# Performance work log

Hardware: AMD Instinct MI355X
Metric: run time of the kernel (lower is better)

The kernel has to match this reference:

```python
import jax, jax.numpy as jnp
import numpy as np

BLOCK = 16
N1, N2, RANK = 64, 64, 64
# E2M1 (NVFP4) representable magnitudes
_FP4_GRID = jnp.array([0.0, 0.5, 1.0, 1.5, 2.0, 3.0, 4.0, 6.0], dtype=jnp.float32)
_FP4_MIDS = (_FP4_GRID[1:] + _FP4_GRID[:-1]) / 2.0


def quantize_to_nvfp4(x, block_size=BLOCK):
    """Per-block (last dim, block_size=16) NVFP4 fake-quant: amax scale to 6.0, round to E2M1 grid, dequant."""
    shape = x.shape
    xb = x.reshape(shape[:-1] + (shape[-1] // block_size, block_size))
    amax = jnp.max(jnp.abs(xb), axis=-1, keepdims=True)
    scale = jnp.maximum(amax / 6.0, 1e-8)
    y = xb / scale
    idx = jnp.searchsorted(_FP4_MIDS, jnp.abs(y), side='right')  # nearest grid index
    q = _FP4_GRID[idx] * jnp.sign(y)
    return (q * scale).reshape(shape)


def setup_inputs() -> dict:
    key = jax.random.key(0)
    ks = jax.random.split(key, 6)
    B, S, n, m, r = 4, 2048, 4096, 4096, RANK
    return {
        'x': jax.random.normal(ks[0], (B, S, n), dtype=jnp.float32),
        'smooth_scale': jax.random.uniform(ks[1], (n,), dtype=jnp.float32, minval=0.2, maxval=2.0),
        'a_q': jax.random.normal(ks[2], (m, r), dtype=jnp.float32) * 0.05,
        'b_q': jax.random.normal(ks[3], (N1, r), dtype=jnp.float32) * 0.1,
        'c_q_t': jax.random.normal(ks[4], (r, N2), dtype=jnp.float32) * 0.1,
        'bias': jax.random.normal(ks[5], (m,), dtype=jnp.float32),
    }


def reference(x, smooth_scale, a_q, b_q, c_q_t, bias):
    # smooth + activation quant
    x_q = quantize_to_nvfp4(x * smooth_scale, BLOCK)
    # reshape (..., n) -> (..., n1, n2)
    x_3d = x_q.reshape(x.shape[:-1] + (N1, N2))
    # contract C: F.linear(x_3d, c_q_t) -> (..., n1, r)
    h1 = jnp.einsum('bsij,rj->bsir', x_3d, c_q_t)
    # contract B: (h1 * B).sum over n1 -> (..., r)
    h2 = jnp.einsum('bsir,ir->bsr', h1, b_q)
    # contract A: h2 @ A.T + bias -> (..., m)
    out = jnp.einsum('bsr,mr->bsm', h2, a_q) + bias
    return out
```

## Files before the change

kernel.cpp:

```cpp
#include <hip/hip_runtime.h>

typedef float f32x4 __attribute__((ext_vector_type(4)));
typedef short s16x8 __attribute__((ext_vector_type(8)));
typedef short s16x4 __attribute__((ext_vector_type(4)));
typedef unsigned short u16;

#define N_COLS 4096
#define RANK 64

__device__ __forceinline__ unsigned f_asuint(float f) { union { float f; unsigned u; } v; v.f = f; return v.u; }
__device__ __forceinline__ float f_asfloat(unsigned u) { union { unsigned u; float f; } v; v.u = u; return v.f; }
__device__ __forceinline__ short f2bf(float f) {
  unsigned u = f_asuint(f);
  return (short)((u + 0x7fffu + ((u >> 16) & 1u)) >> 16);
}

__device__ __forceinline__ void gload_lds16(const void* g, void* l) {
  __builtin_amdgcn_global_load_lds(
      (const __attribute__((address_space(1))) unsigned int*)g,
      (__attribute__((address_space(3))) unsigned int*)l,
      16, 0, 0);
}

__global__ __launch_bounds__(256) void k_prep(const float* __restrict__ b_q,
                                              const float* __restrict__ c_q_t,
                                              const float* __restrict__ a_q,
                                              u16* __restrict__ W,
                                              u16* __restrict__ a_bf) {
  int j = blockIdx.x * 256 + threadIdx.x;
  if (j < 32768) {
    int r = j >> 9;
    int n0 = (j << 3) & 4095;
    float b = b_q[(n0 >> 6) * RANK + r];
    const f32x4* cp = reinterpret_cast<const f32x4*>(c_q_t + (r << 6) + (n0 & 63));
    f32x4 c0 = cp[0], c1 = cp[1];
    s16x8 w;
    w[0] = f2bf(b * c0.x); w[1] = f2bf(b * c0.y); w[2] = f2bf(b * c0.z); w[3] = f2bf(b * c0.w);
    w[4] = f2bf(b * c1.x); w[5] = f2bf(b * c1.y); w[6] = f2bf(b * c1.z); w[7] = f2bf(b * c1.w);
    *reinterpret_cast<s16x8*>(W + ((size_t)j << 3)) = w;
  } else {
    int j2 = j - 32768;
    const f32x4* ap = reinterpret_cast<const f32x4*>(a_q + ((size_t)j2 << 3));
    f32x4 a0 = ap[0], a1 = ap[1];
    s16x8 v;
    v[0] = f2bf(a0.x); v[1] = f2bf(a0.y); v[2] = f2bf(a0.z); v[3] = f2bf(a0.w);
    v[4] = f2bf(a1.x); v[5] = f2bf(a1.y); v[6] = f2bf(a1.z); v[7] = f2bf(a1.w);
    *reinterpret_cast<s16x8*>(a_bf + ((size_t)j2 << 3)) = v;
  }
}

__global__ __launch_bounds__(256, 4) void k_h2(const float* __restrict__ x,
                                               const float* __restrict__ smooth,
                                               const u16* __restrict__ W,
                                               float* __restrict__ h2p,
                                               int T) {
  const int t0 = blockIdx.x * 16;
  const int kb = blockIdx.y;
  const int wave = threadIdx.x >> 6;
  const int lane = threadIdx.x & 63;
  const int quad = lane >> 4;
  const int tl = lane & 15;
  const int K0b = kb << 11;

  __shared__ float xbuf[2][4096];
  __shared__ float sml[2048];

#pragma unroll
  for (int rr = 0; rr < 2; ++rr)
    gload_lds16(smooth + K0b + rr * 1024 + wave * 256 + (lane << 2),
                &sml[rr * 1024 + wave * 256]);

  const int colL = lane << 2;
#pragma unroll
  for (int q = 0; q < 4; ++q) {
    int tok = q * 4 + wave;
    int c = colL ^ ((tok & 7) << 2);
    gload_lds16(x + (size_t)(t0 + tok) * N_COLS + K0b + c, &xbuf[0][tok * 256]);
  }
  __syncthreads();

  f32x4 acc0 = {0.f, 0.f, 0.f, 0.f};
  f32x4 acc1 = {0.f, 0.f, 0.f, 0.f};
  f32x4 acc2 = {0.f, 0.f, 0.f, 0.f};
  f32x4 acc3 = {0.f, 0.f, 0.f, 0.f};

  const int c0w = wave * 64 + quad * 8;
  const int swz = (tl & 7) << 2;
  const u16* wpB = W + (size_t)tl * N_COLS + K0b + c0w;

#pragma unroll
  for (int t = 0; t < 8; ++t) {
    if (t + 1 < 8) {
#pragma unroll
      for (int q = 0; q < 4; ++q) {
        int tok = q * 4 + wave;
        int c = colL ^ ((tok & 7) << 2);
        gload_lds16(x + (size_t)(t0 + tok) * N_COLS + K0b + (t + 1) * 256 + c,
                    &xbuf[(t + 1) & 1][tok * 256]);
      }
    }

    s16x8 w8[2][4];
#pragma unroll
    for (int si = 0; si < 2; ++si)
#pragma unroll
      for (int i = 0; i < 4; ++i)
        w8[si][i] = *reinterpret_cast<const s16x8*>(
            wpB + t * 256 + si * 32 + (size_t)i * 16 * N_COLS);

    const float* xb = xbuf[t & 1];
#pragma unroll
    for (int si = 0; si < 2; ++si) {
      const int cs = c0w + si * 32;
      f32x4 xa = *reinterpret_cast<const f32x4*>(xb + tl * 256 + (cs ^ swz));
      f32x4 xv = *reinterpret_cast<const f32x4*>(xb + tl * 256 + ((cs + 4) ^ swz));
      f32x4 sa = *reinterpret_cast<const f32x4*>(sml + t * 256 + cs);
      f32x4 sb = *reinterpret_cast<const f32x4*>(sml + t * 256 + cs + 4);

      float xs[8];
      xs[0] = xa.x * sa.x; xs[1] = xa.y * sa.y; xs[2] = xa.z * sa.z; xs[3] = xa.w * sa.w;
      xs[4] = xv.x * sb.x; xs[5] = xv.y * sb.y; xs[6] = xv.z * sb.z; xs[7] = xv.w * sb.w;

      float amax = fabsf(xs[0]);
#pragma unroll
      for (int j = 1; j < 8; ++j) amax = fmaxf(amax, fabsf(xs[j]));
      amax = fmaxf(amax, __shfl_xor(amax, 16));
      float scale = fmaxf(amax * (1.0f / 6.0f), 1e-8f);

      const float th0 = 0.25f * scale, th1 = 0.75f * scale, th2 = 1.25f * scale,
                  th3 = 1.75f * scale, th4 = 2.5f * scale, th5 = 3.5f * scale,
                  th6 = 5.0f * scale;
      s16x8 af;
#pragma unroll
      for (int j = 0; j < 8; ++j) {
        float ax = fabsf(xs[j]);
        float q = (ax >= th0) ? 0.5f : 0.0f;
        q = (ax >= th1) ? 1.0f : q;
        q = (ax >= th2) ? 1.5f : q;
        q = (ax >= th3) ? 2.0f : q;
        q = (ax >= th4) ? 3.0f : q;
        q = (ax >= th5) ? 4.0f : q;
        q = (ax >= th6) ? 6.0f : q;
        float xq = q * scale;
        xq = f_asfloat(f_asuint(xq) | (f_asuint(xs[j]) & 0x80000000u));
        af[j] = f2bf(xq);
      }

      acc0 = __builtin_amdgcn_mfma_f32_16x16x32_bf16(af, w8[si][0], acc0, 0, 0, 0);
      acc1 = __builtin_amdgcn_mfma_f32_16x16x32_bf16(af, w8[si][1], acc1, 0, 0, 0);
      acc2 = __builtin_amdgcn_mfma_f32_16x16x32_bf16(af, w8[si][2], acc2, 0, 0, 0);
      acc3 = __builtin_amdgcn_mfma_f32_16x16x32_bf16(af, w8[si][3], acc3, 0, 0, 0);
    }
    __syncthreads();
  }

  float* red = &xbuf[0][0];
  float* rw = red + wave * 1024 + (quad * 4) * 64 + tl;
#pragma unroll
  for (int reg = 0; reg < 4; ++reg) {
    rw[reg * 64 + 0]  = acc0[reg];
    rw[reg * 64 + 16] = acc1[reg];
    rw[reg * 64 + 32] = acc2[reg];
    rw[reg * 64 + 48] = acc3[reg];
  }
  __syncthreads();
  {
    const f32x4* r4 = reinterpret_cast<const f32x4*>(red);
    f32x4 v = r4[threadIdx.x];
#pragma unroll
    for (int p = 1; p < 4; ++p) {
      f32x4 u = r4[p * 256 + threadIdx.x];
      v.x += u.x; v.y += u.y; v.z += u.z; v.w += u.w;
    }
    int t = threadIdx.x >> 4;
    int rr = (threadIdx.x & 15) * 4;
    *reinterpret_cast<f32x4*>(h2p + ((size_t)kb * T + t0 + t) * RANK + rr) = v;
  }
}

__global__ __launch_bounds__(256, 4) void k_gemm2(const float* __restrict__ h2p,
                                                  const u16* __restrict__ a_bf,
                                                  const float* __restrict__ bias,
                                                  float* __restrict__ out,
                                                  int T) {
  const int t0 = blockIdx.y * 32;
  const int m0 = blockIdx.x * 256;
  const int wave = threadIdx.x >> 6;
  const int lane = threadIdx.x & 63;
  const int quad = lane >> 4;
  const int tl = lane & 15;

  __shared__ u16 h2l[32 * 72];
  __shared__ float tile[16 * 260];

  {
    int t = threadIdx.x >> 3;
    int r0 = (threadIdx.x & 7) * 8;
    const float* p = h2p + (size_t)(t0 + t) * RANK + r0;
    f32x4 v0 = *reinterpret_cast<const f32x4*>(p);
    f32x4 v1 = *reinterpret_cast<const f32x4*>(p + 4);
    const float* q = p + (size_t)T * RANK;
    f32x4 u0 = *reinterpret_cast<const f32x4*>(q);
    f32x4 u1 = *reinterpret_cast<const f32x4*>(q + 4);
    v0.x += u0.x; v0.y += u0.y; v0.z += u0.z; v0.w += u0.w;
    v1.x += u1.x; v1.y += u1.y; v1.z += u1.z; v1.w += u1.w;
    s16x8 h;
    h[0] = f2bf(v0.x); h[1] = f2bf(v0.y); h[2] = f2bf(v0.z); h[3] = f2bf(v0.w);
    h[4] = f2bf(v1.x); h[5] = f2bf(v1.y); h[6] = f2bf(v1.z); h[7] = f2bf(v1.w);
    *reinterpret_cast<s16x8*>(h2l + t * 72 + r0) = h;
  }
  __syncthreads();

  const u16* hp0 = h2l + tl * 72 + quad * 8;
  const u16* hp1 = hp0 + 16 * 72;
  const u16* ap = a_bf + (size_t)(m0 + wave * 64 + tl) * RANK + quad * 8;

  f32x4 acc[2][4] = {};

#pragma unroll
  for (int o = 0; o < 64; o += 32) {
    s16x8 a0 = *reinterpret_cast<const s16x8*>(hp0 + o);
    s16x8 a1 = *reinterpret_cast<const s16x8*>(hp1 + o);
#pragma unroll
    for (int mg = 0; mg < 4; ++mg) {
      s16x8 bfr = *reinterpret_cast<const s16x8*>(ap + (size_t)mg * 16 * RANK + o);
      acc[0][mg] = __builtin_amdgcn_mfma_f32_16x16x32_bf16(a0, bfr, acc[0][mg], 0, 0, 0);
      acc[1][mg] = __builtin_amdgcn_mfma_f32_16x16x32_bf16(a1, bfr, acc[1][mg], 0, 0, 0);
    }
  }

#pragma unroll
  for (int tg = 0; tg < 2; ++tg) {
    if (tg) __syncthreads();
#pragma unroll
    for (int mg = 0; mg < 4; ++mg)
#pragma unroll
      for (int reg = 0; reg < 4; ++reg)
        tile[(quad * 4 + reg) * 260 + wave * 64 + mg * 16 + tl] = acc[tg][mg][reg];
    __syncthreads();
#pragma unroll
    for (int i = 0; i < 4; ++i) {
      int idx = threadIdx.x + i * 256;
      int row = idx >> 6;
      int c4 = (idx & 63) << 2;
      f32x4 v = *reinterpret_cast<const f32x4*>(tile + row * 260 + c4);
      f32x4 b = *reinterpret_cast<const f32x4*>(bias + m0 + c4);
      f32x4 ov;
      ov.x = v.x + b.x; ov.y = v.y + b.y; ov.z = v.z + b.z; ov.w = v.w + b.w;
      __builtin_nontemporal_store(ov,
        reinterpret_cast<f32x4*>(out + (size_t)(t0 + tg * 16 + row) * N_COLS + m0 + c4));
    }
  }
}

extern "C" void kernel_launch(void* const* d_in, const int* in_sizes, int n_in,
                              void* d_out, int out_size, void* d_ws, size_t ws_size,
                              hipStream_t stream) {
  const float* x      = (const float*)d_in[0];
  const float* smooth = (const float*)d_in[1];
  const float* a_q    = (const float*)d_in[2];
  const float* b_q    = (const float*)d_in[3];
  const float* c_q_t  = (const float*)d_in[4];
  const float* bias   = (const float*)d_in[5];
  float* out = (float*)d_out;

  const int T = in_sizes[0] / N_COLS;

  u16* W     = (u16*)d_ws;
  u16* a_bf  = (u16*)((char*)d_ws + 524288);
  float* h2p = (float*)((char*)d_ws + 1048576);

  k_prep<<<256, 256, 0, stream>>>(b_q, c_q_t, a_q, W, a_bf);
  dim3 gh(T / 16, 2);
  k_h2<<<gh, 256, 0, stream>>>(x, smooth, W, h2p, T);
  dim3 g2(N_COLS / 256, T / 32);
  k_gemm2<<<g2, 256, 0, stream>>>(h2p, a_bf, bias, out, T);
}
```

Baseline: 262.8 us.

## Fuse rank-projection and output GEMM into one kernel per token tile

Merges the h2 reduction kernel and the output GEMM into a single kernel. Each block processes all 4096 input columns for 16 tokens, keeps h2 in LDS as bf16, then loops over 16 output column chunks writing results with bias. This removes the split-K partial buffer round trip and one kernel launch. The trade-off is fewer blocks (T/16) with lower occupancy and serial output writes per block.

```diff
diff --git a/kernel.cpp b/kernel.cpp
--- a/kernel.cpp
+++ b/kernel.cpp
@@ -49,25 +49,28 @@
   }
 }
 
-__global__ __launch_bounds__(256, 4) void k_h2(const float* __restrict__ x,
-                                               const float* __restrict__ smooth,
-                                               const u16* __restrict__ W,
-                                               float* __restrict__ h2p,
-                                               int T) {
+__global__ __launch_bounds__(256, 2) void k_fused(const float* __restrict__ x,
+                                                  const float* __restrict__ smooth,
+                                                  const u16* __restrict__ W,
+                                                  const u16* __restrict__ a_bf,
+                                                  const float* __restrict__ bias,
+                                                  float* __restrict__ out) {
   const int t0 = blockIdx.x * 16;
-  const int kb = blockIdx.y;
   const int wave = threadIdx.x >> 6;
   const int lane = threadIdx.x & 63;
   const int quad = lane >> 4;
   const int tl = lane & 15;
-  const int K0b = kb << 11;
-
-  __shared__ float xbuf[2][4096];
-  __shared__ float sml[2048];
-
-#pragma unroll
-  for (int rr = 0; rr < 2; ++rr)
-    gload_lds16(smooth + K0b + rr * 1024 + wave * 256 + (lane << 2),
+
+  __shared__ float shmem[8192];
+  __shared__ float sml[4096];
+  __shared__ u16 h2l[16 * 72];
+
+  float* xbuf0 = shmem;
+  float* xbuf1 = shmem + 4096;
+
+#pragma unroll
+  for (int rr = 0; rr < 4; ++rr)
+    gload_lds16(smooth + rr * 1024 + wave * 256 + (lane << 2),
                 &sml[rr * 1024 + wave * 256]);
 
   const int colL = lane << 2;
@@ -75,7 +78,7 @@
   for (int q = 0; q < 4; ++q) {
     int tok = q * 4 + wave;
     int c = colL ^ ((tok & 7) << 2);
-    gload_lds16(x + (size_t)(t0 + tok) * N_COLS + K0b + c, &xbuf[0][tok * 256]);
+    gload_lds16(x + (size_t)(t0 + tok) * N_COLS + c, &xbuf0[tok * 256]);
   }
   __syncthreads();
 
@@ -86,17 +89,18 @@
 
   const int c0w = wave * 64 + quad * 8;
   const int swz = (tl & 7) << 2;
-  const u16* wpB = W + (size_t)tl * N_COLS + K0b + c0w;
-
-#pragma unroll
-  for (int t = 0; t < 8; ++t) {
-    if (t + 1 < 8) {
+  const u16* wpB = W + (size_t)tl * N_COLS + c0w;
+
+#pragma unroll
+  for (int t = 0; t < 16; ++t) {
+    if (t + 1 < 16) {
+      float* nb = ((t + 1) & 1) ? xbuf1 : xbuf0;
 #pragma unroll
       for (int q = 0; q < 4; ++q) {
         int tok = q * 4 + wave;
         int c = colL ^ ((tok & 7) << 2);
-        gload_lds16(x + (size_t)(t0 + tok) * N_COLS + K0b + (t + 1) * 256 + c,
-                    &xbuf[(t + 1) & 1][tok * 256]);
+        gload_lds16(x + (size_t)(t0 + tok) * N_COLS + (t + 1) * 256 + c,
+                    &nb[tok * 256]);
       }
     }
 
@@ -108,7 +112,7 @@
         w8[si][i] = *reinterpret_cast<const s16x8*>(
             wpB + t * 256 + si * 32 + (size_t)i * 16 * N_COLS);
 
-    const float* xb = xbuf[t & 1];
+    const float* xb = (t & 1) ? xbuf1 : xbuf0;
 #pragma unroll
     for (int si = 0; si < 2; ++si) {
       const int cs = c0w + si * 32;
@@ -154,7 +158,7 @@
     __syncthreads();
   }
 
-  float* red = &xbuf[0][0];
+  float* red = xbuf0;
   float* rw = red + wave * 1024 + (quad * 4) * 64 + tl;
 #pragma unroll
   for (int reg = 0; reg < 4; ++reg) {
@@ -174,70 +178,37 @@
     }
     int t = threadIdx.x >> 4;
     int rr = (threadIdx.x & 15) * 4;
-    *reinterpret_cast<f32x4*>(h2p + ((size_t)kb * T + t0 + t) * RANK + rr) = v;
-  }
-}
-
-__global__ __launch_bounds__(256, 4) void k_gemm2(const float* __restrict__ h2p,
-                                                  const u16* __restrict__ a_bf,
-                                                  const float* __restrict__ bias,
-                                                  float* __restrict__ out,
-                                                  int T) {
-  const int t0 = blockIdx.y * 32;
-  const int m0 = blockIdx.x * 256;
-  const int wave = threadIdx.x >> 6;
-  const int lane = threadIdx.x & 63;
-  const int quad = lane >> 4;
-  const int tl = lane & 15;
-
-  __shared__ u16 h2l[32 * 72];
-  __shared__ float tile[16 * 260];
-
-  {
-    int t = threadIdx.x >> 3;
-    int r0 = (threadIdx.x & 7) * 8;
-    const float* p = h2p + (size_t)(t0 + t) * RANK + r0;
-    f32x4 v0 = *reinterpret_cast<const f32x4*>(p);
-    f32x4 v1 = *reinterpret_cast<const f32x4*>(p + 4);
-    const float* q = p + (size_t)T * RANK;
-    f32x4 u0 = *reinterpret_cast<const f32x4*>(q);
-    f32x4 u1 = *reinterpret_cast<const f32x4*>(q + 4);
-    v0.x += u0.x; v0.y += u0.y; v0.z += u0.z; v0.w += u0.w;
-    v1.x += u1.x; v1.y += u1.y; v1.z += u1.z; v1.w += u1.w;
-    s16x8 h;
-    h[0] = f2bf(v0.x); h[1] = f2bf(v0.y); h[2] = f2bf(v0.z); h[3] = f2bf(v0.w);
-    h[4] = f2bf(v1.x); h[5] = f2bf(v1.y); h[6] = f2bf(v1.z); h[7] = f2bf(v1.w);
-    *reinterpret_cast<s16x8*>(h2l + t * 72 + r0) = h;
+    s16x4 o4;
+    o4[0] = f2bf(v.x); o4[1] = f2bf(v.y); o4[2] = f2bf(v.z); o4[3] = f2bf(v.w);
+    *reinterpret_cast<s16x4*>(h2l + t * 72 + rr) = o4;
   }
   __syncthreads();
 
-  const u16* hp0 = h2l + tl * 72 + quad * 8;
-  const u16* hp1 = hp0 + 16 * 72;
-  const u16* ap = a_bf + (size_t)(m0 + wave * 64 + tl) * RANK + quad * 8;
-
-  f32x4 acc[2][4] = {};
-
-#pragma unroll
-  for (int o = 0; o < 64; o += 32) {
-    s16x8 a0 = *reinterpret_cast<const s16x8*>(hp0 + o);
-    s16x8 a1 = *reinterpret_cast<const s16x8*>(hp1 + o);
+  s16x8 h0 = *reinterpret_cast<const s16x8*>(h2l + tl * 72 + quad * 8);
+  s16x8 h1 = *reinterpret_cast<const s16x8*>(h2l + tl * 72 + quad * 8 + 32);
+
+  float* tile = shmem;
+
+  for (int mc = 0; mc < 16; ++mc) {
+    const int m0 = mc * 256;
+    f32x4 acc[4] = {{0.f,0.f,0.f,0.f},{0.f,0.f,0.f,0.f},{0.f,0.f,0.f,0.f},{0.f,0.f,0.f,0.f}};
 #pragma unroll
     for (int mg = 0; mg < 4; ++mg) {
-      s16x8 bfr = *reinterpret_cast<const s16x8*>(ap + (size_t)mg * 16 * RANK + o);
-      acc[0][mg] = __builtin_amdgcn_mfma_f32_16x16x32_bf16(a0, bfr, acc[0][mg], 0, 0, 0);
-      acc[1][mg] = __builtin_amdgcn_mfma_f32_16x16x32_bf16(a1, bfr, acc[1][mg], 0, 0, 0);
-    }
-  }
-
-#pragma unroll
-  for (int tg = 0; tg < 2; ++tg) {
-    if (tg) __syncthreads();
+      const u16* ap = a_bf + (size_t)(m0 + wave * 64 + mg * 16 + tl) * RANK + quad * 8;
+      s16x8 b0 = *reinterpret_cast<const s16x8*>(ap);
+      s16x8 b1 = *reinterpret_cast<const s16x8*>(ap + 32);
+      acc[mg] = __builtin_amdgcn_mfma_f32_16x16x32_bf16(h0, b0, acc[mg], 0, 0, 0);
+      acc[mg] = __builtin_amdgcn_mfma_f32_16x16x32_bf16(h1, b1, acc[mg], 0, 0, 0);
+    }
+
+    __syncthreads();
 #pragma unroll
     for (int mg = 0; mg < 4; ++mg)
 #pragma unroll
       for (int reg = 0; reg < 4; ++reg)
-        tile[(quad * 4 + reg) * 260 + wave * 64 + mg * 16 + tl] = acc[tg][mg][reg];
+        tile[(quad * 4 + reg) * 260 + wave * 64 + mg * 16 + tl] = acc[mg][reg];
     __syncthreads();
+
 #pragma unroll
     for (int i = 0; i < 4; ++i) {
       int idx = threadIdx.x + i * 256;
@@ -248,7 +219,7 @@
       f32x4 ov;
       ov.x = v.x + b.x; ov.y = v.y + b.y; ov.z = v.z + b.z; ov.w = v.w + b.w;
       __builtin_nontemporal_store(ov,
-        reinterpret_cast<f32x4*>(out + (size_t)(t0 + tg * 16 + row) * N_COLS + m0 + c4));
+        reinterpret_cast<f32x4*>(out + (size_t)(t0 + row) * N_COLS + m0 + c4));
     }
   }
 }
@@ -266,13 +237,9 @@
 
   const int T = in_sizes[0] / N_COLS;
 
-  u16* W     = (u16*)d_ws;
-  u16* a_bf  = (u16*)((char*)d_ws + 524288);
-  float* h2p = (float*)((char*)d_ws + 1048576);
+  u16* W    = (u16*)d_ws;
+  u16* a_bf = (u16*)((char*)d_ws + 524288);
 
   k_prep<<<256, 256, 0, stream>>>(b_q, c_q_t, a_q, W, a_bf);
-  dim3 gh(T / 16, 2);
-  k_h2<<<gh, 256, 0, stream>>>(x, smooth, W, h2p, T);
-  dim3 g2(N_COLS / 256, T / 32);
-  k_gemm2<<<g2, 256, 0, stream>>>(h2p, a_bf, bias, out, T);
-}
+  k_fused<<<T / 16, 256, 0, stream>>>(x, smooth, W, a_bf, bias, out);
+}
```

Result: slower. 273.2 us (+4.0%).
